# Kernel optimization log

Measured on AMD Instinct MI355X. Metric: run time of the kernel, lower is better.

Reference implementation:

```python
import jax, jax.numpy as jnp
import numpy as np

B, N, F_IN, H, D = 2, 3000, 64, 4, 32
NEG = -1e9  # mask value used by the original layer

def setup_inputs() -> dict:
    key = jax.random.key(0)
    ks = jax.random.split(key, 6)
    h = jax.random.normal(ks[0], (B, N, F_IN), dtype=jnp.float32)
    # dense 0/1 adjacency
    a = jax.random.randint(ks[1], (B, N, N), 0, 2).astype(jnp.float32)
    kernel = jax.random.normal(ks[2], (H, F_IN, D), dtype=jnp.float32) * 0.1
    att_k1 = jax.random.normal(ks[3], (H, D), dtype=jnp.float32) * 0.1
    att_k2 = jax.random.normal(ks[4], (H, D), dtype=jnp.float32) * 0.1
    bias = jax.random.normal(ks[5], (H, D), dtype=jnp.float32) * 0.1
    return {"h": h, "a": a, "kernel": kernel, "att_k1": att_k1, "att_k2": att_k2, "bias": bias}

def reference(h, a, kernel, att_k1, att_k2, bias):
    # per-head projection: [B,H,N,D]
    feat = jnp.einsum('bnf,hfd->bhnd', h, kernel)
    e1 = jnp.einsum('bhnd,hd->bhn', feat, att_k1)  # attention (query part)
    e2 = jnp.einsum('bhnd,hd->bhn', feat, att_k2)  # attention_2 (key part)
    # dense branch: att = a * (e1_i + e2_j); NO LeakyReLU in dense path (faithful)
    adj = a[:, None]                                   # [B,1,N,N]
    scores = adj * (e1[..., :, None] + e2[..., None, :])
    scores = scores + jnp.where(adj == 0, jnp.float32(NEG), jnp.float32(0))
    att = jax.nn.softmax(scores, axis=-1)
    att = att * (adj != 0).astype(att.dtype)
    # dropout is identity at inference
    out = jnp.einsum('bhnm,bhmd->bhnd', att, feat)
    out = out + bias[None, :, None, :]
    out = jax.nn.relu(out)
    # zero out all-zero input nodes
    node_mask = (jnp.sum((h != 0).astype(jnp.float32), axis=-1, keepdims=True) > 0).astype(jnp.float32)  # [B,N,1]
    out = out * node_mask[:, None]
    # concat heads -> [B,N,H*D]
    return out.transpose(0, 2, 1, 3).reshape(h.shape[0], h.shape[1], -1)
```

## Files before the change

kernel.cpp:

```cpp
#include <hip/hip_runtime.h>
#include <hip/hip_bf16.h>
#include <stdint.h>

#define B_ 2
#define N_ 3000
#define F_ 64
#define H_ 4
#define D_ 32
#define K_ 128
#define KT_ 9
#define NCH_ 94
#define NROWT_ 188

typedef short bf16x8 __attribute__((ext_vector_type(8)));
typedef float f32x4  __attribute__((ext_vector_type(4)));

__device__ __forceinline__ unsigned short f2bf(float f) {
    uint32_t x = __float_as_uint(f);
    return (unsigned short)((x + 0x7FFFu + ((x >> 16) & 1u)) >> 16);
}

__global__ void k_feat(const float* __restrict__ hin, const float* __restrict__ kern,
                       const float* __restrict__ ak2,
                       float* __restrict__ feat, float* __restrict__ e2,
                       float* __restrict__ nmask) {
    int b = blockIdx.x / N_;
    int n = blockIdx.x % N_;
    __shared__ float hrow[F_];
    int tid = threadIdx.x;
    if (tid < F_) hrow[tid] = hin[(size_t)(b * N_ + n) * F_ + tid];
    __syncthreads();
    int hh = tid >> 5, d = tid & 31;
    float acc = 0.f;
    #pragma unroll
    for (int f = 0; f < F_; ++f)
        acc = fmaf(hrow[f], kern[(hh * F_ + f) * D_ + d], acc);
    feat[((size_t)(b * H_ + hh) * N_ + n) * D_ + d] = acc;
    float v = acc * ak2[hh * D_ + d];
    #pragma unroll
    for (int o = 16; o >= 1; o >>= 1) v += __shfl_xor(v, o, 32);
    if (d == 0) e2[(size_t)(b * H_ + hh) * N_ + n] = v;
    unsigned long long bal = __ballot(tid < F_ && hrow[tid & (F_ - 1)] != 0.0f);
    if (tid == 0) nmask[b * N_ + n] = (bal != 0ull) ? 1.0f : 0.0f;
}

__global__ void k_G(const float* __restrict__ feat, const float* __restrict__ e2,
                    bf16x8* __restrict__ G) {
    int idx = blockIdx.x * blockDim.x + threadIdx.x;
    const int total = B_ * NCH_ * KT_ * 64;
    if (idx >= total) return;
    int lane = idx & 63;
    int t  = (idx >> 6) % KT_;
    int ch = ((idx >> 6) / KT_) % NCH_;
    int b  = idx / (64 * KT_ * NCH_);
    int rg = lane >> 4, col = lane & 15;
    int k  = t * 16 + col;
    int m0 = ch * 32 + rg * 8;
    float vals[8];
    if (k < K_ + H_) {
        int hh, d; bool wonly;
        if (k < K_) { hh = k >> 5; d = k & 31; wonly = false; }
        else        { hh = k - K_; d = 0;      wonly = true;  }
        const float* e2p = e2 + (size_t)(b * H_ + hh) * N_;
        const float* fp  = feat + (size_t)(b * H_ + hh) * N_ * D_ + d;
        #pragma unroll
        for (int j = 0; j < 8; ++j) {
            int m = m0 + j;
            float v = 0.f;
            if (m < N_) {
                float w = __expf(e2p[m]);
                v = wonly ? w : w * fp[(size_t)m * D_];
            }
            vals[j] = v;
        }
    } else {
        #pragma unroll
        for (int j = 0; j < 8; ++j) vals[j] = 0.f;
    }
    union { bf16x8 v; unsigned short u[8]; } o;
    #pragma unroll
    for (int j = 0; j < 8; ++j) o.u[j] = f2bf(vals[j]);
    G[idx] = o.v;
}

__device__ __forceinline__ void loadsetA(const float* __restrict__ arow, int ch, int rg,
                                         f32x4& f0, f32x4& f1) {
    if (ch == NCH_ - 1 && rg == 3) {
        f0 = (f32x4){0.f, 0.f, 0.f, 0.f};
        f1 = (f32x4){0.f, 0.f, 0.f, 0.f};
    } else {
        const f32x4* p = (const f32x4*)(arow + ch * 32 + rg * 8);
        f0 = p[0]; f1 = p[1];
    }
}

__device__ __forceinline__ void loadsetG(const bf16x8* __restrict__ Gb, int ch,
                                         bf16x8 (&g)[KT_]) {
    const bf16x8* p = Gb + (size_t)ch * KT_ * 64;
    #pragma unroll
    for (int t = 0; t < KT_; ++t) g[t] = p[t * 64];
}

__device__ __forceinline__ void computeset(const f32x4& f0, const f32x4& f1,
                                           const bf16x8 (&g)[KT_], f32x4 (&acc)[KT_]) {
    union { uint32_t u[4]; bf16x8 v; } af;
    af.u[0] = ((f0.x != 0.f) ? 0x3F80u : 0u) | ((f0.y != 0.f) ? 0x3F800000u : 0u);
    af.u[1] = ((f0.z != 0.f) ? 0x3F80u : 0u) | ((f0.w != 0.f) ? 0x3F800000u : 0u);
    af.u[2] = ((f1.x != 0.f) ? 0x3F80u : 0u) | ((f1.y != 0.f) ? 0x3F800000u : 0u);
    af.u[3] = ((f1.z != 0.f) ? 0x3F80u : 0u) | ((f1.w != 0.f) ? 0x3F800000u : 0u);
    #pragma unroll
    for (int t = 0; t < KT_; ++t)
        acc[t] = __builtin_amdgcn_mfma_f32_16x16x32_bf16(af.v, g[t], acc[t], 0, 0, 0);
}

__global__ void __launch_bounds__(256) k_main(
        const float* __restrict__ a, const bf16x8* __restrict__ G,
        const float* __restrict__ bias, const float* __restrict__ nmask,
        float* __restrict__ out) {
    int blk = blockIdx.x;
    int b  = blk / NROWT_;
    int rt = blk % NROWT_;
    int nbase = rt * 16;
    int w = threadIdx.x >> 6;
    int l = threadIdx.x & 63;
    int rg = l >> 4, col = l & 15;
    int arow_i = nbase + col;
    int aclamp = min(arow_i, N_ - 1);
    const float* arow = a + (size_t)(b * N_ + aclamp) * N_;
    const bf16x8* Gb = G + (size_t)b * NCH_ * KT_ * 64 + l;

    int c0 = (w < 2) ? w * 24 : 48 + (w - 2) * 23;
    int c1 = c0 + ((w < 2) ? 24 : 23);

    f32x4 acc[KT_];
    #pragma unroll
    for (int t = 0; t < KT_; ++t) acc[t] = (f32x4){0.f, 0.f, 0.f, 0.f};

    f32x4 aA0, aA1, aB0, aB1;
    bf16x8 gA[KT_], gB[KT_];
    loadsetA(arow, c0, rg, aA0, aA1);
    loadsetG(Gb, c0, gA);
    int ch = c0;
    for (;;) {
        if (ch + 1 < c1) { loadsetA(arow, ch + 1, rg, aB0, aB1); loadsetG(Gb, ch + 1, gB); }
        computeset(aA0, aA1, gA, acc);
        if (++ch >= c1) break;
        if (ch + 1 < c1) { loadsetA(arow, ch + 1, rg, aA0, aA1); loadsetG(Gb, ch + 1, gA); }
        computeset(aB0, aB1, gB, acc);
        if (++ch >= c1) break;
    }

    __shared__ float red[4][KT_ * 4][64];
    __shared__ float dl[16][4];
    #pragma unroll
    for (int t = 0; t < KT_; ++t)
        #pragma unroll
        for (int r = 0; r < 4; ++r)
            red[w][t * 4 + r][l] = acc[t][r];
    __syncthreads();

    if (threadIdx.x < 64) {
        int rowi = threadIdx.x >> 2;
        int hh   = threadIdx.x & 3;
        int rg2 = rowi >> 2, r2 = rowi & 3;
        int lane2 = (rg2 << 4) | hh;
        dl[rowi][hh] = red[0][32 + r2][lane2] + red[1][32 + r2][lane2]
                     + red[2][32 + r2][lane2] + red[3][32 + r2][lane2];
    }
    __syncthreads();

    #pragma unroll
    for (int i = 0; i < 8; ++i) {
        int t4r = w + i * 4;
        int t = t4r >> 2, r = t4r & 3;
        int rowi = rg * 4 + r;
        int n = nbase + rowi;
        if (n < N_) {
            float s = red[0][t4r][l] + red[1][t4r][l] + red[2][t4r][l] + red[3][t4r][l];
            int hh = t >> 1;
            float den = dl[rowi][hh];
            float v = (den > 0.f) ? s / den : 0.f;
            v += bias[t * 16 + col];
            v = fmaxf(v, 0.f);
            v *= nmask[b * N_ + n];
            out[(size_t)(b * N_ + n) * K_ + t * 16 + col] = v;
        }
    }
}

extern "C" void kernel_launch(void* const* d_in, const int* in_sizes, int n_in,
                              void* d_out, int out_size, void* d_ws, size_t ws_size,
                              hipStream_t stream) {
    const float* h    = (const float*)d_in[0];
    const float* a    = (const float*)d_in[1];
    const float* kern = (const float*)d_in[2];
    const float* ak2  = (const float*)d_in[4];
    const float* bias = (const float*)d_in[5];
    float* out = (float*)d_out;

    char* ws = (char*)d_ws;
    size_t o_feat  = 0;
    size_t o_e2    = o_feat  + 3072000;
    size_t o_nmask = o_e2    + 96000;
    size_t o_G     = o_nmask + 24064;
    float*  feat  = (float*)(ws + o_feat);
    float*  e2    = (float*)(ws + o_e2);
    float*  nmask = (float*)(ws + o_nmask);
    bf16x8* G     = (bf16x8*)(ws + o_G);

    k_feat<<<dim3(B_ * N_), dim3(128), 0, stream>>>(h, kern, ak2, feat, e2, nmask);
    int gtot = B_ * NCH_ * KT_ * 64;
    k_G   <<<dim3((gtot + 255) / 256), dim3(256), 0, stream>>>(feat, e2, G);
    k_main<<<dim3(B_ * NROWT_), dim3(256), 0, stream>>>(a, G, bias, nmask, out);
}
```

Measured before the change: 49.80 us.

## Split main kernel along key dimension and add separate reduction kernel

Splits the N-dimension (key chunks) of the aggregation GEMM across 8 blocks per row tile, so 3008 blocks run instead of 376. Each block writes its partial sums to workspace, and a new reduction kernel adds them and applies the normalisation, bias, ReLU and node mask. The goal is more parallelism and better memory-bandwidth use when streaming the adjacency matrix. The cost is an extra kernel launch plus partial-sum traffic of about 27 MB written and read back.

```diff
diff --git a/kernel.cpp b/kernel.cpp
--- a/kernel.cpp
+++ b/kernel.cpp
@@ -11,6 +11,8 @@
 #define KT_ 9
 #define NCH_ 94
 #define NROWT_ 188
+#define S_ 8
+#define PT_ 2304
 
 typedef short bf16x8 __attribute__((ext_vector_type(8)));
 typedef float f32x4  __attribute__((ext_vector_type(4)));
@@ -113,13 +115,13 @@
         acc[t] = __builtin_amdgcn_mfma_f32_16x16x32_bf16(af.v, g[t], acc[t], 0, 0, 0);
 }
 
-__global__ void __launch_bounds__(256) k_main(
+__global__ void __launch_bounds__(256, 2) k_main(
         const float* __restrict__ a, const bf16x8* __restrict__ G,
-        const float* __restrict__ bias, const float* __restrict__ nmask,
-        float* __restrict__ out) {
-    int blk = blockIdx.x;
-    int b  = blk / NROWT_;
-    int rt = blk % NROWT_;
+        float* __restrict__ partial) {
+    int bid = blockIdx.x;
+    int s  = bid % S_;
+    int rt = (bid / S_) % NROWT_;
+    int b  = bid / (S_ * NROWT_);
     int nbase = rt * 16;
     int w = threadIdx.x >> 6;
     int l = threadIdx.x & 63;
@@ -129,8 +131,10 @@
     const float* arow = a + (size_t)(b * N_ + aclamp) * N_;
     const bf16x8* Gb = G + (size_t)b * NCH_ * KT_ * 64 + l;
 
-    int c0 = (w < 2) ? w * 24 : 48 + (w - 2) * 23;
-    int c1 = c0 + ((w < 2) ? 24 : 23);
+    int g0 = (s * NCH_) / S_, g1 = ((s + 1) * NCH_) / S_;
+    int len = g1 - g0;
+    int c0 = g0 + (w * len) / 4;
+    int c1 = g0 + ((w + 1) * len) / 4;
 
     f32x4 acc[KT_];
     #pragma unroll
@@ -151,39 +155,59 @@
     }
 
     __shared__ float red[4][KT_ * 4][64];
-    __shared__ float dl[16][4];
     #pragma unroll
     for (int t = 0; t < KT_; ++t)
         #pragma unroll
         for (int r = 0; r < 4; ++r)
             red[w][t * 4 + r][l] = acc[t][r];
     __syncthreads();
-
-    if (threadIdx.x < 64) {
-        int rowi = threadIdx.x >> 2;
-        int hh   = threadIdx.x & 3;
-        int rg2 = rowi >> 2, r2 = rowi & 3;
-        int lane2 = (rg2 << 4) | hh;
-        dl[rowi][hh] = red[0][32 + r2][lane2] + red[1][32 + r2][lane2]
-                     + red[2][32 + r2][lane2] + red[3][32 + r2][lane2];
+    float* pout = partial + (size_t)bid * PT_;
+    #pragma unroll
+    for (int k = 0; k < 9; ++k) {
+        int flat = threadIdx.x + k * 256;
+        int x = flat >> 6, y = flat & 63;
+        pout[flat] = red[0][x][y] + red[1][x][y] + red[2][x][y] + red[3][x][y];
+    }
+}
+
+__global__ void __launch_bounds__(256) k_red(
+        const float* __restrict__ partial, const float* __restrict__ bias,
+        const float* __restrict__ nmask, float* __restrict__ out) {
+    int rt = blockIdx.x % NROWT_;
+    int b  = blockIdx.x / NROWT_;
+    int nbase = rt * 16;
+    int tid = threadIdx.x;
+    __shared__ float sm[PT_];
+    const float* pbase = partial + (size_t)((b * NROWT_ + rt) * S_) * PT_;
+    #pragma unroll
+    for (int k = 0; k < 9; ++k) {
+        int flat = tid + k * 256;
+        float s = 0.f;
+        #pragma unroll
+        for (int sp = 0; sp < S_; ++sp) s += pbase[(size_t)sp * PT_ + flat];
+        sm[flat] = s;
     }
     __syncthreads();
-
-    #pragma unroll
-    for (int i = 0; i < 8; ++i) {
-        int t4r = w + i * 4;
-        int t = t4r >> 2, r = t4r & 3;
-        int rowi = rg * 4 + r;
-        int n = nbase + rowi;
-        if (n < N_) {
-            float s = red[0][t4r][l] + red[1][t4r][l] + red[2][t4r][l] + red[3][t4r][l];
-            int hh = t >> 1;
-            float den = dl[rowi][hh];
-            float v = (den > 0.f) ? s / den : 0.f;
-            v += bias[t * 16 + col];
-            v = fmaxf(v, 0.f);
-            v *= nmask[b * N_ + n];
-            out[(size_t)(b * N_ + n) * K_ + t * 16 + col] = v;
+    #pragma unroll
+    for (int k = 0; k < 9; ++k) {
+        int flat = tid + k * 256;
+        if (flat < 2048) {
+            int t4r = flat >> 6;
+            int t = t4r >> 2, r = t4r & 3;
+            int lane = flat & 63;
+            int rg = lane >> 4, col = lane & 15;
+            int rowi = rg * 4 + r;
+            int n = nbase + rowi;
+            if (n < N_) {
+                int hh = t >> 1;
+                int r2 = rowi & 3, rg2 = rowi >> 2;
+                float den = sm[(32 + r2) * 64 + (rg2 << 4) + hh];
+                float v = (den > 0.f) ? sm[flat] / den : 0.f;
+                v += bias[t * 16 + col];
+                v = fmaxf(v, 0.f);
+                v *= nmask[b * N_ + n];
+                out[(size_t)(b * N_ + n) * K_ + t * 16 + col] = v;
+            }
         }
     }
 }
@@ -203,13 +227,16 @@
     size_t o_e2    = o_feat  + 3072000;
     size_t o_nmask = o_e2    + 96000;
     size_t o_G     = o_nmask + 24064;
+    size_t o_part  = o_G     + 1732608;
     float*  feat  = (float*)(ws + o_feat);
     float*  e2    = (float*)(ws + o_e2);
     float*  nmask = (float*)(ws + o_nmask);
     bf16x8* G     = (bf16x8*)(ws + o_G);
+    float*  part  = (float*)(ws + o_part);
 
     k_feat<<<dim3(B_ * N_), dim3(128), 0, stream>>>(h, kern, ak2, feat, e2, nmask);
     int gtot = B_ * NCH_ * KT_ * 64;
     k_G   <<<dim3((gtot + 255) / 256), dim3(256), 0, stream>>>(feat, e2, G);
-    k_main<<<dim3(B_ * NROWT_), dim3(256), 0, stream>>>(a, G, bias, nmask, out);
-}
+    k_main<<<dim3(B_ * NROWT_ * S_), dim3(256), 0, stream>>>(a, G, part);
+    k_red <<<dim3(B_ * NROWT_), dim3(256), 0, stream>>>(part, bias, nmask, out);
+}
```

Result: slower. 53.36 us (+7.1%).
